# Kernel tuning notes

Measured on AMD Instinct MI355X. Metric: run time of the kernel, lower is better.

## Reference

```python
import jax, jax.numpy as jnp
import numpy as np

HEADS = 16
EPS = 1e-12


def setup_inputs() -> dict:
    key = jax.random.key(0)
    ks = jax.random.split(key, 5)
    B, S, H = 4, 2048, 1024
    scale = 1.0 / np.sqrt(H)
    return {
        "input": jax.random.normal(ks[0], (B, S, H), jnp.float32),
        "input_mask": jnp.zeros((B, 1, 1, S), jnp.float32),  # additive mask
        "norm_w": jnp.ones((H,), jnp.float32),
        "norm_b": jnp.zeros((H,), jnp.float32),
        "attn_qkvw": jax.random.normal(ks[1], (3 * H, H), jnp.float32) * scale,
        "attn_qkvb": jax.random.normal(ks[2], (3 * H,), jnp.float32) * 0.01,
        "attn_ow": jax.random.normal(ks[3], (H, H), jnp.float32) * scale,
    }


def reference(input, input_mask, norm_w, norm_b, attn_qkvw, attn_qkvb, attn_ow):
    B, S, H = input.shape
    d_head = H // HEADS

    # qkv_gemm: fused LayerNorm + QKV projection (pre_layer_norm path)
    mu = jnp.mean(input, axis=-1, keepdims=True)
    var = jnp.mean(jnp.square(input - mu), axis=-1, keepdims=True)
    ln = (input - mu) * jax.lax.rsqrt(var + EPS) * norm_w + norm_b
    qkv = ln @ attn_qkvw.T + attn_qkvb  # [B,S,3H]

    q, k, v = jnp.split(qkv, 3, axis=-1)  # each [B,S,H]
    key_layer, value_layer = k, v  # returned pre-transpose, as in the fused path

    qh = q.reshape(B, S, HEADS, d_head).transpose(0, 2, 1, 3)  # [B,h,S,d]
    kh = k.reshape(B, S, HEADS, d_head).transpose(0, 2, 1, 3)
    vh = v.reshape(B, S, HEADS, d_head).transpose(0, 2, 1, 3)

    # fused softmax-attention: score scale nets to 1/sqrt(d_head)
    scores = jnp.einsum("bhqd,bhkd->bhqk", qh, kh) / jnp.sqrt(
        jnp.asarray(d_head, input.dtype)) + input_mask
    p = jax.nn.softmax(scores, axis=-1)
    ctx = jnp.einsum("bhqk,bhkd->bhqd", p, vh)  # [B,h,S,d]
    context_layer = ctx.transpose(0, 2, 1, 3).reshape(B, S, H)

    # vector_matmul output projection (bias added outside this module)
    output = context_layer @ attn_ow.T
    return (output, key_layer, value_layer, context_layer)
```

## Files before the change

kernel.cpp:

```cpp
#include <hip/hip_runtime.h>
#include <cstdint>


typedef __attribute__((ext_vector_type(8))) short short8;
typedef __attribute__((ext_vector_type(4))) short short4v;
typedef __attribute__((ext_vector_type(4))) float floatx4;

#define BSH 8388608
#define PART_STRIDE 8388608
#define LOG2E 1.4426950408889634f

static __device__ __forceinline__ short f2bf(float f) {
  union { float f; uint32_t u; } v; v.f = f;
  uint32_t r = v.u + 0x7fffu + ((v.u >> 16) & 1u);
  return (short)(r >> 16);
}
static __device__ __forceinline__ short f2bf_fast(float f) {
  union { float f; uint32_t u; } v; v.f = f;
  return (short)((v.u + 0x8000u) >> 16);
}

typedef __attribute__((address_space(1))) void gas_t;
typedef __attribute__((address_space(3))) void las_t;
static __device__ __forceinline__ void async16(const void* g, const void* l) {
  __builtin_amdgcn_global_load_lds((gas_t*)(uintptr_t)g,
                                   (las_t*)(uint32_t)(uintptr_t)l, 16, 0, 0);
}

__global__ __launch_bounds__(256) void k_convert(const float4* __restrict__ wqkv,
                                                 const float4* __restrict__ ow,
                                                 short4v* __restrict__ dq,
                                                 short4v* __restrict__ dow) {
  const int n1 = (3072 * 1024) / 4, n2 = (1024 * 1024) / 4;
  for (int i = blockIdx.x * 256 + threadIdx.x; i < n1 + n2; i += gridDim.x * 256) {
    float4 v = (i < n1) ? wqkv[i] : ow[i - n1];
    short4v s;
    s[0] = f2bf(v.x); s[1] = f2bf(v.y); s[2] = f2bf(v.z); s[3] = f2bf(v.w);
    if (i < n1) dq[i] = s; else dow[i - n1] = s;
  }
}

__global__ __launch_bounds__(256) void k_ln(const float* __restrict__ x,
                                            const float* __restrict__ w,
                                            const float* __restrict__ bb,
                                            short* __restrict__ out) {
  const int row = blockIdx.x, t = threadIdx.x;
  float4 v = ((const float4*)(x + row * 1024))[t];
  float s = v.x + v.y + v.z + v.w;
  float sq = v.x * v.x + v.y * v.y + v.z * v.z + v.w * v.w;
#pragma unroll
  for (int off = 32; off; off >>= 1) { s += __shfl_down(s, off); sq += __shfl_down(sq, off); }
  __shared__ float ls[4], lq[4];
  if ((t & 63) == 0) { ls[t >> 6] = s; lq[t >> 6] = sq; }
  __syncthreads();
  s = ls[0] + ls[1] + ls[2] + ls[3];
  sq = lq[0] + lq[1] + lq[2] + lq[3];
  float mu = s * (1.0f / 1024.0f);
  float var = sq * (1.0f / 1024.0f) - mu * mu;
  float rs = rsqrtf(fmaxf(var, 0.0f) + 1e-12f);
  float4 wv = ((const float4*)w)[t];
  float4 bv = ((const float4*)bb)[t];
  short4v o;
  o[0] = f2bf((v.x - mu) * rs * wv.x + bv.x);
  o[1] = f2bf((v.y - mu) * rs * wv.y + bv.y);
  o[2] = f2bf((v.z - mu) * rs * wv.z + bv.z);
  o[3] = f2bf((v.w - mu) * rs * wv.w + bv.w);
  ((short4v*)out)[row * 256 + t] = o;
}

template <int MODE>
__global__ __launch_bounds__(256) void k_gemm(const short* __restrict__ A,
                                              const short* __restrict__ Bm,
                                              const float* __restrict__ bias,
                                              float* __restrict__ out,
                                              short* __restrict__ qkvh,
                                              int K, int N) {
  __shared__ short As[128 * 32], Bs[128 * 32];
  const int tid = threadIdx.x, lane = tid & 63, w = tid >> 6;
  const int quad = lane >> 4, l15 = lane & 15;
  const int wr = w >> 1, wc = w & 1;
  const int m0 = blockIdx.y * 128, n0 = blockIdx.x * 128;
  floatx4 acc[4][4] = {};
  for (int k0 = 0; k0 < K; k0 += 32) {
    __syncthreads();
#pragma unroll
    for (int r = 0; r < 2; r++) {
      int pb = r * 256 + w * 64;
      int p = pb + lane;
      int row = p >> 2, c = (p & 3) ^ ((p >> 3) & 3);
      async16(&A[(m0 + row) * K + k0 + c * 8], &As[pb * 8]);
      async16(&Bm[(n0 + row) * K + k0 + c * 8], &Bs[pb * 8]);
    }
    __syncthreads();
    short8 af[4], bf[4];
#pragma unroll
    for (int i = 0; i < 4; i++) {
      int ar = wr * 64 + i * 16 + l15;
      af[i] = *(const short8*)&As[ar * 32 + ((quad ^ ((ar >> 1) & 3)) * 8)];
      int br = wc * 64 + i * 16 + l15;
      bf[i] = *(const short8*)&Bs[br * 32 + ((quad ^ ((br >> 1) & 3)) * 8)];
    }
#pragma unroll
    for (int i = 0; i < 4; i++)
#pragma unroll
      for (int j = 0; j < 4; j++)
        acc[i][j] = __builtin_amdgcn_mfma_f32_16x16x32_bf16(af[i], bf[j], acc[i][j], 0, 0, 0);
  }
  const int grB = m0 + wr * 64, gcB = n0 + wc * 64;
  const float QS = 0.125f * LOG2E;
#pragma unroll
  for (int i = 0; i < 4; i++) {
#pragma unroll
    for (int j = 0; j < 4; j++) {
      int gc = gcB + j * 16 + l15;
      if (MODE == 0) {
        float bv = bias[gc];
        int part = gc >> 10, within = gc & 1023;
        int head = within >> 6, dd = within & 63;
#pragma unroll
        for (int reg = 0; reg < 4; reg++) {
          int gr = grB + i * 16 + quad * 4 + reg;
          float val = acc[i][j][reg] + bv;
          int b_ = gr >> 11, s_ = gr & 2047;
          int hs = (b_ * 16 + head);
          if (part == 0) {
            qkvh[(hs * 2048 + s_) * 64 + dd] = f2bf(val * QS);
          } else if (part == 1) {
            qkvh[PART_STRIDE + (hs * 2048 + s_) * 64 + dd] = f2bf(val);
            out[BSH + gr * 1024 + within] = val;
          } else {
            out[2 * BSH + gr * 1024 + within] = val;
          }
        }
      } else {
#pragma unroll
        for (int reg = 0; reg < 4; reg++) {
          int gr = grB + i * 16 + quad * 4 + reg;
          out[gr * N + gc] = acc[i][j][reg];
        }
      }
    }
  }
}

__global__ __launch_bounds__(256) void k_vt(const float* __restrict__ vsrc,
                                            short* __restrict__ vt) {
  const int st = blockIdx.x, h = blockIdx.y, b = blockIdx.z;
  const int t = threadIdx.x;
  __shared__ short Ls[64 * 64];
  const int s0 = st * 64;
#pragma unroll
  for (int j = 0; j < 4; j++) {
    int flat = j * 1024 + t * 4;
    int sl = flat >> 6, d = flat & 63;
    float4 v4 = *(const float4*)&vsrc[(size_t)(b * 2048 + s0 + sl) * 1024 + h * 64 + d];
    short4v s4;
    s4[0] = f2bf(v4.x); s4[1] = f2bf(v4.y); s4[2] = f2bf(v4.z); s4[3] = f2bf(v4.w);
    *(short4v*)&Ls[sl * 64 + (((d >> 3) ^ (sl & 7)) * 8) + (d & 7)] = s4;
  }
  __syncthreads();
  const int d = t >> 2, sbase = (t & 3) * 16;
#pragma unroll
  for (int half = 0; half < 2; half++) {
    short8 o;
#pragma unroll
    for (int j = 0; j < 8; j++) {
      int s = sbase + half * 8 + j;
      o[j] = Ls[s * 64 + (((d >> 3) ^ (s & 7)) * 8) + (d & 7)];
    }
    *(short8*)&vt[(size_t)((b * 16 + h) * 64 + d) * 2048 + s0 + sbase + half * 8] = o;
  }
}

__global__ __launch_bounds__(256, 3) void k_attn(const short* __restrict__ qkvh,
                                                 const float* __restrict__ mask,
                                                 float* __restrict__ ctx_out,
                                                 short* __restrict__ ctx_bf) {
  const int qt = blockIdx.x, h = blockIdx.y, b = blockIdx.z;
  const int tid = threadIdx.x, lane = tid & 63, w = tid >> 6;
  const int quad = lane >> 4, l15 = lane & 15;
  __shared__ short Ks[2][64 * 64];
  __shared__ short Vt[2][64 * 64];
  __shared__ short Pl[4][32 * 64];
  const short* qg = qkvh + (size_t)(b * 16 + h) * 2048 * 64;
  const short* kg = qg + PART_STRIDE;
  const short* vg = qkvh + 2 * PART_STRIDE + (size_t)(b * 16 + h) * 64 * 2048;
  const float* mb = mask + b * 2048;

  short8 qf[2][2];
#pragma unroll
  for (int rt = 0; rt < 2; rt++) {
    const int qr = qt * 128 + w * 32 + rt * 16 + l15;
#pragma unroll
    for (int ks = 0; ks < 2; ks++)
      qf[rt][ks] = *(const short8*)&qg[qr * 64 + ks * 32 + quad * 8];
  }

  short8 ones;
#pragma unroll
  for (int j = 0; j < 8; j++) ones[j] = (short)0x3F80;

  floatx4 accO[2][4] = {};
  floatx4 accL[2] = {};

  auto stage = [&](int kt, int bi) {
#pragma unroll
    for (int r = 0; r < 2; r++) {
      int pb = r * 256 + w * 64;
      int p = pb + lane;
      int row = p >> 3, c = (p & 7) ^ (row & 7);
      async16(&kg[(kt * 64 + row) * 64 + c * 8], &Ks[bi][pb * 8]);
      async16(&vg[row * 2048 + kt * 64 + c * 8], &Vt[bi][pb * 8]);
    }
  };
  stage(0, 0);

  for (int kt = 0; kt < 32; kt++) {
    const int cur = kt & 1;
    __syncthreads();
    if (kt + 1 < 32) stage(kt + 1, cur ^ 1);

    float mv[4][4];
#pragma unroll
    for (int nt = 0; nt < 4; nt++) {
      float4 t = *(const float4*)&mb[kt * 64 + nt * 16 + quad * 4];
      mv[nt][0] = t.x; mv[nt][1] = t.y; mv[nt][2] = t.z; mv[nt][3] = t.w;
    }

    floatx4 sc[2][4] = {};
#pragma unroll
    for (int nt = 0; nt < 4; nt++) {
      const int krow = nt * 16 + l15;
#pragma unroll
      for (int ks = 0; ks < 2; ks++) {
        short8 kf = *(const short8*)&Ks[cur][krow * 64 + (((ks * 4 + quad) ^ (krow & 7)) * 8)];
        sc[0][nt] = __builtin_amdgcn_mfma_f32_16x16x32_bf16(kf, qf[0][ks], sc[0][nt], 0, 0, 0);
        sc[1][nt] = __builtin_amdgcn_mfma_f32_16x16x32_bf16(kf, qf[1][ks], sc[1][nt], 0, 0, 0);
      }
    }

#pragma unroll
    for (int rt = 0; rt < 2; rt++) {
      const int qb = rt * 16 + l15;
      const int base = qb * 64 + (quad & 1) * 4;
      const int sw = qb & 7;
#pragma unroll
      for (int nt = 0; nt < 4; nt++) {
        const int v = nt * 2 + (quad >> 1);
        short4v p4;
#pragma unroll
        for (int reg = 0; reg < 4; reg++)
          p4[reg] = f2bf_fast(__builtin_amdgcn_exp2f(
              fmaf(mv[nt][reg], LOG2E, sc[rt][nt][reg])));
        *(short4v*)&Pl[w][base + ((v ^ sw) * 8)] = p4;
      }
    }

#pragma unroll
    for (int ks2 = 0; ks2 < 2; ks2++) {
      short8 pf[2];
#pragma unroll
      for (int rt = 0; rt < 2; rt++) {
        const int prow = rt * 16 + l15;
        pf[rt] = *(const short8*)&Pl[w][prow * 64 + (((ks2 * 4 + quad) ^ (prow & 7)) * 8)];
        accL[rt] = __builtin_amdgcn_mfma_f32_16x16x32_bf16(pf[rt], ones, accL[rt], 0, 0, 0);
      }
#pragma unroll
      for (int nt2 = 0; nt2 < 4; nt2++) {
        const int vrow = nt2 * 16 + l15;
        short8 vf = *(const short8*)&Vt[cur][vrow * 64 + (((ks2 * 4 + quad) ^ (vrow & 7)) * 8)];
        accO[0][nt2] = __builtin_amdgcn_mfma_f32_16x16x32_bf16(pf[0], vf, accO[0][nt2], 0, 0, 0);
        accO[1][nt2] = __builtin_amdgcn_mfma_f32_16x16x32_bf16(pf[1], vf, accO[1][nt2], 0, 0, 0);
      }
    }
  }

#pragma unroll
  for (int rt = 0; rt < 2; rt++) {
    float inv[4];
#pragma unroll
    for (int reg = 0; reg < 4; reg++) inv[reg] = 1.0f / accL[rt][reg];
#pragma unroll
    for (int nt2 = 0; nt2 < 4; nt2++)
#pragma unroll
      for (int reg = 0; reg < 4; reg++) {
        const int qrow = qt * 128 + w * 32 + rt * 16 + quad * 4 + reg;
        const int col = h * 64 + nt2 * 16 + l15;
        const int gi = (b * 2048 + qrow) * 1024 + col;
        float val = accO[rt][nt2][reg] * inv[reg];
        ctx_out[gi] = val;
        ctx_bf[gi] = f2bf(val);
      }
  }
}

extern "C" void kernel_launch(void* const* d_in, const int* in_sizes, int n_in,
                              void* d_out, int out_size, void* d_ws, size_t ws_size,
                              hipStream_t stream) {
  const float* x    = (const float*)d_in[0];
  const float* mask = (const float*)d_in[1];
  const float* nw   = (const float*)d_in[2];
  const float* nb   = (const float*)d_in[3];
  const float* wqkv = (const float*)d_in[4];
  const float* bqkv = (const float*)d_in[5];
  const float* ow   = (const float*)d_in[6];
  float* out = (float*)d_out;
  char* ws = (char*)d_ws;

  short* lnb   = (short*)ws;
  short* wqkvb = (short*)(ws + 16777216);
  short* owb   = (short*)(ws + 23068672);
  short* qkvh  = (short*)(ws + 25165824);
  short* vt    = qkvh + 2 * (size_t)PART_STRIDE;

  k_convert<<<512, 256, 0, stream>>>((const float4*)wqkv, (const float4*)ow,
                                     (short4v*)wqkvb, (short4v*)owb);
  k_ln<<<8192, 256, 0, stream>>>(x, nw, nb, lnb);
  k_gemm<0><<<dim3(24, 64), 256, 0, stream>>>(lnb, wqkvb, bqkv, out, qkvh, 1024, 3072);
  k_vt<<<dim3(32, 16, 4), 256, 0, stream>>>(out + 2 * (size_t)BSH, vt);
  k_attn<<<dim3(16, 16, 4), 256, 0, stream>>>(qkvh, mask, out + 3 * (size_t)BSH, lnb);
  k_gemm<1><<<dim3(8, 64), 256, 0, stream>>>(lnb, owb, nullptr, out, nullptr, 1024, 1024);
}
```

Before: 405.8 us.

## Keep attention probabilities in registers via permlane swaps instead of LDS round-trip

The exponentiated scores are now packed to bf16 with v_cvt_pk_bf16_f32 and rearranged across lanes with v_permlane32/16_swap, so they form the MFMA A-operand directly. This removes the per-wave LDS staging buffer for P along with its write and read traffic. Freeing that LDS and raising the launch-bounds occupancy hint from 3 to 4 blocks per CU should increase concurrency. The risks are more register pressure under the tighter bound, and the lane permutation must map exactly onto the MFMA operand layout. Rounding also changes from the custom round-half-up to the hardware conversion.

```diff
diff --git a/kernel.cpp b/kernel.cpp
--- a/kernel.cpp
+++ b/kernel.cpp
@@ -14,10 +14,6 @@
   union { float f; uint32_t u; } v; v.f = f;
   uint32_t r = v.u + 0x7fffu + ((v.u >> 16) & 1u);
   return (short)(r >> 16);
-}
-static __device__ __forceinline__ short f2bf_fast(float f) {
-  union { float f; uint32_t u; } v; v.f = f;
-  return (short)((v.u + 0x8000u) >> 16);
 }
 
 typedef __attribute__((address_space(1))) void gas_t;
@@ -25,6 +21,24 @@
 static __device__ __forceinline__ void async16(const void* g, const void* l) {
   __builtin_amdgcn_global_load_lds((gas_t*)(uintptr_t)g,
                                    (las_t*)(uint32_t)(uintptr_t)l, 16, 0, 0);
+}
+
+static __device__ __forceinline__ uint32_t cvt_pk_bf16(float a, float b) {
+  uint32_t r;
+  asm("v_cvt_pk_bf16_f32 %0, %1, %2" : "=v"(r) : "v"(a), "v"(b));
+  return r;
+}
+static __device__ __forceinline__ void swap32(uint32_t& a, uint32_t& b) {
+  asm("v_permlane32_swap_b32 %0, %1" : "+v"(a), "+v"(b));
+}
+static __device__ __forceinline__ void swap16(uint32_t& a, uint32_t& b) {
+  asm("v_permlane16_swap_b32 %0, %1" : "+v"(a), "+v"(b));
+}
+static __device__ __forceinline__ short8 s8_from(uint32_t a, uint32_t b,
+                                                 uint32_t c, uint32_t d) {
+  union { uint32_t u[4]; short8 s; } t;
+  t.u[0] = a; t.u[1] = b; t.u[2] = c; t.u[3] = d;
+  return t.s;
 }
 
 __global__ __launch_bounds__(256) void k_convert(const float4* __restrict__ wqkv,
@@ -172,7 +186,7 @@
   }
 }
 
-__global__ __launch_bounds__(256, 3) void k_attn(const short* __restrict__ qkvh,
+__global__ __launch_bounds__(256, 4) void k_attn(const short* __restrict__ qkvh,
                                                  const float* __restrict__ mask,
                                                  float* __restrict__ ctx_out,
                                                  short* __restrict__ ctx_bf) {
@@ -181,7 +195,6 @@
   const int quad = lane >> 4, l15 = lane & 15;
   __shared__ short Ks[2][64 * 64];
   __shared__ short Vt[2][64 * 64];
-  __shared__ short Pl[4][32 * 64];
   const short* qg = qkvh + (size_t)(b * 16 + h) * 2048 * 64;
   const short* kg = qg + PART_STRIDE;
   const short* vg = qkvh + 2 * PART_STRIDE + (size_t)(b * 16 + h) * 64 * 2048;
@@ -239,38 +252,39 @@
       }
     }
 
+    uint32_t pa[2][2][4];
 #pragma unroll
     for (int rt = 0; rt < 2; rt++) {
-      const int qb = rt * 16 + l15;
-      const int base = qb * 64 + (quad & 1) * 4;
-      const int sw = qb & 7;
-#pragma unroll
-      for (int nt = 0; nt < 4; nt++) {
-        const int v = nt * 2 + (quad >> 1);
-        short4v p4;
-#pragma unroll
-        for (int reg = 0; reg < 4; reg++)
-          p4[reg] = f2bf_fast(__builtin_amdgcn_exp2f(
-              fmaf(mv[nt][reg], LOG2E, sc[rt][nt][reg])));
-        *(short4v*)&Pl[w][base + ((v ^ sw) * 8)] = p4;
+#pragma unroll
+      for (int e = 0; e < 2; e++) {
+#pragma unroll
+        for (int d = 0; d < 2; d++) {
+          float p0 = __builtin_amdgcn_exp2f(fmaf(mv[2 * e][2 * d], LOG2E, sc[rt][2 * e][2 * d]));
+          float p1 = __builtin_amdgcn_exp2f(fmaf(mv[2 * e][2 * d + 1], LOG2E, sc[rt][2 * e][2 * d + 1]));
+          float p2 = __builtin_amdgcn_exp2f(fmaf(mv[2 * e + 1][2 * d], LOG2E, sc[rt][2 * e + 1][2 * d]));
+          float p3 = __builtin_amdgcn_exp2f(fmaf(mv[2 * e + 1][2 * d + 1], LOG2E, sc[rt][2 * e + 1][2 * d + 1]));
+          uint32_t rE = cvt_pk_bf16(p0, p1);
+          uint32_t rO = cvt_pk_bf16(p2, p3);
+          swap32(rE, rO);
+          swap16(rE, rO);
+          pa[rt][e][d] = rE;
+          pa[rt][e][2 + d] = rO;
+        }
       }
     }
 
 #pragma unroll
     for (int ks2 = 0; ks2 < 2; ks2++) {
-      short8 pf[2];
-#pragma unroll
-      for (int rt = 0; rt < 2; rt++) {
-        const int prow = rt * 16 + l15;
-        pf[rt] = *(const short8*)&Pl[w][prow * 64 + (((ks2 * 4 + quad) ^ (prow & 7)) * 8)];
-        accL[rt] = __builtin_amdgcn_mfma_f32_16x16x32_bf16(pf[rt], ones, accL[rt], 0, 0, 0);
-      }
+      short8 pf0 = s8_from(pa[0][ks2][0], pa[0][ks2][1], pa[0][ks2][2], pa[0][ks2][3]);
+      short8 pf1 = s8_from(pa[1][ks2][0], pa[1][ks2][1], pa[1][ks2][2], pa[1][ks2][3]);
+      accL[0] = __builtin_amdgcn_mfma_f32_16x16x32_bf16(pf0, ones, accL[0], 0, 0, 0);
+      accL[1] = __builtin_amdgcn_mfma_f32_16x16x32_bf16(pf1, ones, accL[1], 0, 0, 0);
 #pragma unroll
       for (int nt2 = 0; nt2 < 4; nt2++) {
         const int vrow = nt2 * 16 + l15;
         short8 vf = *(const short8*)&Vt[cur][vrow * 64 + (((ks2 * 4 + quad) ^ (vrow & 7)) * 8)];
-        accO[0][nt2] = __builtin_amdgcn_mfma_f32_16x16x32_bf16(pf[0], vf, accO[0][nt2], 0, 0, 0);
-        accO[1][nt2] = __builtin_amdgcn_mfma_f32_16x16x32_bf16(pf[1], vf, accO[1][nt2], 0, 0, 0);
+        accO[0][nt2] = __builtin_amdgcn_mfma_f32_16x16x32_bf16(pf0, vf, accO[0][nt2], 0, 0, 0);
+        accO[1][nt2] = __builtin_amdgcn_mfma_f32_16x16x32_bf16(pf1, vf, accO[1][nt2], 0, 0, 0);
       }
     }
   }
```

Result: faster. 385.5 us (-5.0%).
